# Performance work log

Measured on AMD Instinct MI355X. Metric: run time of the kernel, lower is better.

## Reference

```python
import jax, jax.numpy as jnp
import numpy as np

S, W, V, E, P, PD, H = 2048, 96, 100000, 100, 4096, 50, 100


def setup_inputs() -> dict:
    key = jax.random.key(0)
    ks = jax.random.split(key, 12)
    # small scale (0.05) on params keeps sigmoid/tanh out of saturation
    return {
        "x": jax.random.randint(ks[0], (S, W), 0, V, dtype=jnp.int64) if jax.config.read("jax_enable_x64") else jax.random.randint(ks[0], (S, W), 0, V, dtype=jnp.int32),
        "word_emb": jax.random.normal(ks[1], (V, E), jnp.float32) * 0.05,
        "pos_emb": jax.random.normal(ks[2], (P, PD), jnp.float32) * 0.05,
        "fc1_w": jax.random.normal(ks[3], (H, H), jnp.float32) * 0.05,
        "fc1_b": jax.random.normal(ks[4], (H,), jnp.float32) * 0.05,
        "fc2_w": jax.random.normal(ks[5], (H, H), jnp.float32) * 0.05,
        "fc2_b": jax.random.normal(ks[6], (H,), jnp.float32) * 0.05,
        "Wc": jax.random.normal(ks[7], (1, H), jnp.float32) * 0.05,
        "Ws": jax.random.normal(ks[8], (H, H), jnp.float32) * 0.05,
        "Wr": jax.random.normal(ks[9], (H, H), jnp.float32) * 0.05,
        "Wp": jax.random.normal(ks[10], (1, PD), jnp.float32) * 0.05,
        "b": jax.random.normal(ks[11], (1,), jnp.float32) * 0.05,
    }


def reference(x, word_emb, pos_emb, fc1_w, fc1_b, fc2_w, fc2_b, Wc, Ws, Wr, Wp, b):
    # ragged avg pooling: length = count of nonzero tokens; torch slices data[:length]
    lengths = jnp.sum(jnp.sign(x), axis=1)                     # (S,)
    we = word_emb[x]                                           # (S,W,E)
    mask = (jnp.arange(W)[None, :] < lengths[:, None]).astype(we.dtype)
    denom = jnp.maximum(lengths, 1).astype(we.dtype)[:, None]
    sent = (we * mask[..., None]).sum(axis=1) / denom          # (S,E)

    doc_feat = sent.mean(axis=0)                               # (E,)
    doc = jnp.tanh(doc_feat @ fc1_w.T + fc1_b)                 # (H,)

    h = jnp.tanh(sent @ fc2_w.T + fc2_b)                       # (S,H)
    pos = pos_emb[jnp.arange(S)]                               # (S,PD)

    # per-sentence logit pieces independent of recurrent state s
    pre = h @ Wc[0] + (h @ Ws) @ doc + pos @ Wp[0] + b[0]      # (S,)
    hWr = h @ Wr                                               # (S,H)

    def step(s, inp):
        hi, hwri, prei = inp
        logit = prei - hwri @ jnp.tanh(s)
        prob = jax.nn.sigmoid(logit)
        return s + hi * prob, prob

    s0 = jnp.zeros((H,), h.dtype)
    _, probs = jax.lax.scan(step, s0, (h, hWr, pre))
    return probs[:, None]                                      # (S,1)
```

## Files before the change

kernel.cpp:

```cpp
#include <hip/hip_runtime.h>
#include <hip/hip_bf16.h>

#define S 2048
#define W 96
#define E 100
#define H 100
#define PD 50

typedef float f32x4 __attribute__((ext_vector_type(4)));

__device__ __forceinline__ float fast_rcp(float x) { return __builtin_amdgcn_rcpf(x); }

template<int CTRL, int RM, bool BND>
__device__ __forceinline__ float dpp_add(float x) {
    int t = __builtin_amdgcn_update_dpp(0, __float_as_int(x), CTRL, RM, 0xf, BND);
    return x + __int_as_float(t);
}

__device__ __forceinline__ float wave_sum_bcast(float x) {
    x = dpp_add<0x111, 0xf, true >(x);
    x = dpp_add<0x112, 0xf, true >(x);
    x = dpp_add<0x114, 0xf, true >(x);
    x = dpp_add<0x118, 0xf, true >(x);
    x = dpp_add<0x142, 0xa, false>(x);
    x = dpp_add<0x143, 0xc, false>(x);
    return __int_as_float(__builtin_amdgcn_readlane(__float_as_int(x), 63));
}

__global__ __launch_bounds__(128) void k_sent(const int* __restrict__ x,
                                              const float* __restrict__ word_emb,
                                              float* __restrict__ sent,
                                              float* __restrict__ doc_sum) {
    __shared__ int toks[W];
    __shared__ int s_len;
    const int i = blockIdx.x, t = threadIdx.x;
    if (t == 0) s_len = 0;
    __syncthreads();
    if (t < W) {
        int tok = x[i * W + t];
        toks[t] = tok;
        if (tok > 0) atomicAdd(&s_len, 1);
    }
    __syncthreads();
    const int len = s_len;
    if (t < E) {
        float acc = 0.0f;
        for (int j = 0; j < len; ++j)
            acc += word_emb[toks[j] * E + t];
        float val = acc / (float)max(len, 1);
        sent[i * E + t] = val;
        atomicAdd(&doc_sum[t], val * (1.0f / (float)S));
    }
}

__global__ __launch_bounds__(128) void k_doc(const float* __restrict__ doc_sum,
                                             const float* __restrict__ fc1_w,
                                             const float* __restrict__ fc1_b,
                                             const float* __restrict__ Wc,
                                             const float* __restrict__ Ws,
                                             float* __restrict__ cvec) {
    __shared__ float s_df[E];
    __shared__ float s_doc[H];
    const int t = threadIdx.x;
    if (t < E) s_df[t] = doc_sum[t];
    __syncthreads();
    if (t < H) {
        float acc = fc1_b[t];
        for (int k = 0; k < E; ++k) acc += s_df[k] * fc1_w[t * E + k];
        s_doc[t] = tanhf(acc);
    }
    __syncthreads();
    if (t < H) {
        float c = Wc[t];
        for (int j = 0; j < H; ++j) c += Ws[t * H + j] * s_doc[j];
        cvec[t] = c;
    }
}

__global__ __launch_bounds__(128) void k_row(const float* __restrict__ sent,
                                             const float* __restrict__ fc2_w,
                                             const float* __restrict__ fc2_b,
                                             const float* __restrict__ Wr,
                                             const float* __restrict__ cvec,
                                             const float* __restrict__ pos_emb,
                                             const float* __restrict__ Wp,
                                             const float* __restrict__ bptr,
                                             float* __restrict__ packed) {
    __shared__ float s_sent[E];
    __shared__ float s_h[H];
    __shared__ float red[128];
    const int i = blockIdx.x, t = threadIdx.x;
    float* row = packed + (size_t)i * 256;
    if (t < E) s_sent[t] = sent[i * E + t];
    __syncthreads();
    float hv = 0.0f;
    if (t < H) {
        float acc = fc2_b[t];
        for (int k = 0; k < E; ++k) acc += s_sent[k] * fc2_w[t * E + k];
        hv = tanhf(acc);
        s_h[t] = hv;
    }
    __syncthreads();
    {
        const int m = t >> 1, o = (t & 1) * 2;
        if (t < H) {
            float acc = 0.0f;
            for (int k = 0; k < H; ++k) acc += s_h[k] * Wr[k * H + t];
            row[m * 4 + o]     = 1.44269504f * acc;
            row[m * 4 + o + 1] = hv;
        } else {
            if (t != 100) row[m * 4 + o] = 0.0f;
            row[m * 4 + o + 1] = 0.0f;
        }
    }
    float p = 0.0f;
    if (t < H) p = hv * cvec[t];
    if (t < PD) p += pos_emb[i * PD + t] * Wp[t];
    red[t] = p;
    __syncthreads();
    for (int m = 64; m > 0; m >>= 1) {
        if (t < m) red[t] += red[t + m];
        __syncthreads();
    }
    if (t == 0) row[200] = -1.44269504f * (red[0] + bptr[0]);
}

__global__ __launch_bounds__(64, 1) void k_scan(const f32x4* __restrict__ packed,
                                                float* __restrict__ out) {
    const int l = threadIdx.x;
    const f32x4* pf = packed + l;
    const float mq = (l == 50) ? 1.0f : 0.0f;

    float t0 = 0.0f, t1 = 0.0f, probbuf = 0.0f;

    f32x4 x0, x1, x2, x3, x4, x5, x6, x7;
    f32x4 y0, y1, y2, y3, y4, y5, y6, y7;

#define SB() __builtin_amdgcn_sched_barrier(0)
#define ISSUE(AR, PTR) \
    asm volatile("global_load_dwordx4 %0, %1, off" : "=v"(AR) : "v"(PTR))
#define ISSUE8(P0, P1, P2, P3, P4, P5, P6, P7)                                \
    SB();                                                                     \
    ISSUE(P0, pf + 0 * 64); ISSUE(P1, pf + 1 * 64);                           \
    ISSUE(P2, pf + 2 * 64); ISSUE(P3, pf + 3 * 64);                           \
    ISSUE(P4, pf + 4 * 64); ISSUE(P5, pf + 5 * 64);                           \
    ISSUE(P6, pf + 6 * 64); ISSUE(P7, pf + 7 * 64);                           \
    pf += 8 * 64;                                                             \
    SB();
#define WAIT_ALL()                                                            \
    SB();                                                                     \
    asm volatile("s_waitcnt vmcnt(0)" ::: "memory");                          \
    SB();

#define STEP(CA_, IDX, G)                                                     \
    {                                                                         \
                 \
        float part = fmaf(t0, CA_.x, fmaf(t1, CA_.z, mq * CA_.x));            \
        float total = wave_sum_bcast(part);    \
        float e2 = exp2f(total);                                              \
        float prob = fast_rcp(1.0f + e2);                                     \
         \
        float d0 = CA_.y * prob, d1 = CA_.w * prob;                           \
        float u0 = d0 * d0, u1 = d1 * d1;                                     \
        float T0 = d0 * fmaf(u0, fmaf(u0, 0.13333334f, -0.33333334f), 1.0f);  \
        float T1 = d1 * fmaf(u1, fmaf(u1, 0.13333334f, -0.33333334f), 1.0f);  \
        float r0 = fast_rcp(fmaf(t0, T0, 1.0f));                              \
        float r1 = fast_rcp(fmaf(t1, T1, 1.0f));                              \
        t0 = (t0 + T0) * r0;                                                  \
        t1 = (t1 + T1) * r1;                                                  \
        probbuf = (l == ((G + IDX) & 63)) ? prob : probbuf;                   \
    }
#define COMPUTE8(P0, P1, P2, P3, P4, P5, P6, P7, G)                           \
    STEP(P0, 0, G) STEP(P1, 1, G) STEP(P2, 2, G) STEP(P3, 3, G)               \
    STEP(P4, 4, G) STEP(P5, 5, G) STEP(P6, 6, G) STEP(P7, 7, G)               \
    if (((G) & 63) == 56) out[((G) & ~63) + l] = probbuf;

    ISSUE8(x0, x1, x2, x3, x4, x5, x6, x7)
    WAIT_ALL()

    for (int base = 0; base < S; base += 16) {
        ISSUE8(y0, y1, y2, y3, y4, y5, y6, y7)
        COMPUTE8(x0, x1, x2, x3, x4, x5, x6, x7, base)
        WAIT_ALL()
        ISSUE8(x0, x1, x2, x3, x4, x5, x6, x7)
        COMPUTE8(y0, y1, y2, y3, y4, y5, y6, y7, base + 8)
        WAIT_ALL()
    }
#undef COMPUTE8
#undef STEP
#undef WAIT_ALL
#undef ISSUE8
#undef ISSUE
#undef SB
}

extern "C" void kernel_launch(void* const* d_in, const int* in_sizes, int n_in,
                              void* d_out, int out_size, void* d_ws, size_t ws_size,
                              hipStream_t stream) {
    const int*   x        = (const int*)  d_in[0];
    const float* word_emb = (const float*)d_in[1];
    const float* pos_emb  = (const float*)d_in[2];
    const float* fc1_w    = (const float*)d_in[3];
    const float* fc1_b    = (const float*)d_in[4];
    const float* fc2_w    = (const float*)d_in[5];
    const float* fc2_b    = (const float*)d_in[6];
    const float* Wc       = (const float*)d_in[7];
    const float* Ws       = (const float*)d_in[8];
    const float* Wr       = (const float*)d_in[9];
    const float* Wp       = (const float*)d_in[10];
    const float* bptr     = (const float*)d_in[11];
    float* out = (float*)d_out;

    float* wsf      = (float*)d_ws;
    float* doc_sum  = wsf;
    float* cvec     = wsf + 128;
    float* sent     = wsf + 256;
    float* packed   = sent + S * E;

    hipMemsetAsync(doc_sum, 0, E * sizeof(float), stream);
    hipMemsetAsync(packed + (size_t)S * 256, 0, 16 * 256 * sizeof(float), stream);
    k_sent<<<S, 128, 0, stream>>>(x, word_emb, sent, doc_sum);
    k_doc<<<1, 128, 0, stream>>>(doc_sum, fc1_w, fc1_b, Wc, Ws, cvec);
    k_row<<<S, 128, 0, stream>>>(sent, fc2_w, fc2_b, Wr, cvec, pos_emb, Wp, bptr, packed);
    k_scan<<<1, 64, 0, stream>>>((const f32x4*)packed, out);
}
```

Baseline: 332.7 us.

## Break scan dependency with two-step lookahead linearized logit prediction

Restructures the serial scan so the wave reductions for step i+1 and i+2 are computed one step ahead. The next logit is formed from precomputed reduced terms plus first-order corrections in the current and previous probabilities, taking the cross-lane reduction off the critical path between consecutive steps. It also shortens the tanh series to two terms, stores 1+e2 and inverts once per store, and adds a mid-block vmcnt wait so the lookahead can read the next batch's registers. This trades exactness for a linearized approximation of tanh's derivative and lower-order tanh, which adds numerical risk. The extra wait also reduces overlap of the loads.

```diff
diff --git a/kernel.cpp b/kernel.cpp
--- a/kernel.cpp
+++ b/kernel.cpp
@@ -129,22 +129,25 @@
                                                 float* __restrict__ out) {
     const int l = threadIdx.x;
     const f32x4* pf = packed + l;
-    const float mq = (l == 50) ? 1.0f : 0.0f;
-
-    float t0 = 0.0f, t1 = 0.0f, probbuf = 0.0f;
-
-    f32x4 x0, x1, x2, x3, x4, x5, x6, x7;
-    f32x4 y0, y1, y2, y3, y4, y5, y6, y7;
+
+    float t0 = (l == 50) ? 1.0f : 0.0f;
+    float t1 = 0.0f, probbuf = 1.0f;
+    float p1 = 0.0f, p2 = 0.0f;
+    float hp0 = 0.0f, hp1 = 0.0f;
+    float aE, bE, cE, aO, bO, cO;
+
+    f32x4 a0, a1, a2, a3, a4, a5, a6, a7;
+    f32x4 b0, b1, b2, b3, b4, b5, b6, b7;
 
 #define SB() __builtin_amdgcn_sched_barrier(0)
 #define ISSUE(AR, PTR) \
     asm volatile("global_load_dwordx4 %0, %1, off" : "=v"(AR) : "v"(PTR))
-#define ISSUE8(P0, P1, P2, P3, P4, P5, P6, P7)                                \
+#define ISSUE8(R0, R1, R2, R3, R4, R5, R6, R7)                                \
     SB();                                                                     \
-    ISSUE(P0, pf + 0 * 64); ISSUE(P1, pf + 1 * 64);                           \
-    ISSUE(P2, pf + 2 * 64); ISSUE(P3, pf + 3 * 64);                           \
-    ISSUE(P4, pf + 4 * 64); ISSUE(P5, pf + 5 * 64);                           \
-    ISSUE(P6, pf + 6 * 64); ISSUE(P7, pf + 7 * 64);                           \
+    ISSUE(R0, pf + 0 * 64); ISSUE(R1, pf + 1 * 64);                           \
+    ISSUE(R2, pf + 2 * 64); ISSUE(R3, pf + 3 * 64);                           \
+    ISSUE(R4, pf + 4 * 64); ISSUE(R5, pf + 5 * 64);                           \
+    ISSUE(R6, pf + 6 * 64); ISSUE(R7, pf + 7 * 64);                           \
     pf += 8 * 64;                                                             \
     SB();
 #define WAIT_ALL()                                                            \
@@ -152,41 +155,75 @@
     asm volatile("s_waitcnt vmcnt(0)" ::: "memory");                          \
     SB();
 
-#define STEP(CA_, IDX, G)                                                     \
+#define STEP(CUR, NXT, WP2, AX, BX, CX, IDX, G)                               \
     {                                                                         \
-                 \
-        float part = fmaf(t0, CA_.x, fmaf(t1, CA_.z, mq * CA_.x));            \
-        float total = wave_sum_bcast(part);    \
-        float e2 = exp2f(total);                                              \
-        float prob = fast_rcp(1.0f + e2);                                     \
-         \
-        float d0 = CA_.y * prob, d1 = CA_.w * prob;                           \
+                                    \
+        float tot = fmaf(p1, CX, fmaf(p2, BX, AX));                           \
+        float e2 = exp2f(tot);                                                \
+        float av = e2 + 1.0f;                                                 \
+        float pj = fast_rcp(av);                                              \
+             \
+        float d0 = hp0 * p1, d1 = hp1 * p1;                                   \
         float u0 = d0 * d0, u1 = d1 * d1;                                     \
-        float T0 = d0 * fmaf(u0, fmaf(u0, 0.13333334f, -0.33333334f), 1.0f);  \
-        float T1 = d1 * fmaf(u1, fmaf(u1, 0.13333334f, -0.33333334f), 1.0f);  \
-        float r0 = fast_rcp(fmaf(t0, T0, 1.0f));                              \
-        float r1 = fast_rcp(fmaf(t1, T1, 1.0f));                              \
-        t0 = (t0 + T0) * r0;                                                  \
-        t1 = (t1 + T1) * r1;                                                  \
-        probbuf = (l == ((G + IDX) & 63)) ? prob : probbuf;                   \
-    }
-#define COMPUTE8(P0, P1, P2, P3, P4, P5, P6, P7, G)                           \
-    STEP(P0, 0, G) STEP(P1, 1, G) STEP(P2, 2, G) STEP(P3, 3, G)               \
-    STEP(P4, 4, G) STEP(P5, 5, G) STEP(P6, 6, G) STEP(P7, 7, G)               \
-    if (((G) & 63) == 56) out[((G) & ~63) + l] = probbuf;
-
-    ISSUE8(x0, x1, x2, x3, x4, x5, x6, x7)
+        float T0 = d0 * fmaf(u0, -0.33333334f, 1.0f);                         \
+        float T1 = d1 * fmaf(u1, -0.33333334f, 1.0f);                         \
+        float dM0 = fmaf(t0, T0, 1.0f), dM1 = fmaf(t1, T1, 1.0f);             \
+        t0 = (t0 + T0) * fast_rcp(dM0);                                       \
+        t1 = (t1 + T1) * fast_rcp(dM1);                                       \
+                      \
+        float om0 = fmaf(-t0, t0, 1.0f), om1 = fmaf(-t1, t1, 1.0f);           \
+        float gB0 = CUR.y * om0, gB1 = CUR.w * om1;                           \
+        float gC0 = NXT.y * om0, gC1 = NXT.w * om1;                           \
+        float pA = fmaf(t0, WP2.x, t1 * WP2.z);                               \
+        float pB = fmaf(gB0, WP2.x, gB1 * WP2.z);                             \
+        float pC = fmaf(gC0, WP2.x, gC1 * WP2.z);                             \
+        AX = wave_sum_bcast(pA);                                              \
+        BX = wave_sum_bcast(pB);                                              \
+        CX = wave_sum_bcast(pC);                                              \
+        hp0 = CUR.y; hp1 = CUR.w;                                             \
+        p2 = p1; p1 = pj;                                                     \
+        probbuf = (l == ((G + IDX) & 63)) ? av : probbuf;                     \
+    }
+#define MIDWAIT()                                                             \
+    SB();                                                                     \
+    asm volatile("s_waitcnt vmcnt(0)" ::: "memory");                          \
+    SB();
+#define COMPUTE8(R0, R1, R2, R3, R4, R5, R6, R7, Q0, Q1, G)                   \
+    STEP(R0, R1, R2, aE, bE, cE, 0, G)                                        \
+    STEP(R1, R2, R3, aO, bO, cO, 1, G)                                        \
+    STEP(R2, R3, R4, aE, bE, cE, 2, G)                                        \
+    STEP(R3, R4, R5, aO, bO, cO, 3, G)                                        \
+    STEP(R4, R5, R6, aE, bE, cE, 4, G)                                        \
+    STEP(R5, R6, R7, aO, bO, cO, 5, G)                                        \
+    MIDWAIT()                                                                 \
+    STEP(R6, R7, Q0, aE, bE, cE, 6, G)                                        \
+    STEP(R7, Q0, Q1, aO, bO, cO, 7, G)                                        \
+    if (((G) & 63) == 56) out[((G) & ~63) + l] = fast_rcp(probbuf);
+
+    ISSUE8(a0, a1, a2, a3, a4, a5, a6, a7)
     WAIT_ALL()
 
+    {
+        float pA0 = fmaf(t0, a0.x, t1 * a0.z);
+        aE = wave_sum_bcast(pA0);  bE = 0.0f;  cE = 0.0f;
+        float pA1 = fmaf(t0, a1.x, t1 * a1.z);
+        aO = wave_sum_bcast(pA1);  bO = 0.0f;
+        float om0 = fmaf(-t0, t0, 1.0f), om1 = fmaf(-t1, t1, 1.0f);
+        float g0 = a0.y * om0, g1 = a0.w * om1;
+        float pC1 = fmaf(g0, a1.x, g1 * a1.z);
+        cO = wave_sum_bcast(pC1);
+    }
+
     for (int base = 0; base < S; base += 16) {
-        ISSUE8(y0, y1, y2, y3, y4, y5, y6, y7)
-        COMPUTE8(x0, x1, x2, x3, x4, x5, x6, x7, base)
+        ISSUE8(b0, b1, b2, b3, b4, b5, b6, b7)
+        COMPUTE8(a0, a1, a2, a3, a4, a5, a6, a7, b0, b1, base)
         WAIT_ALL()
-        ISSUE8(x0, x1, x2, x3, x4, x5, x6, x7)
-        COMPUTE8(y0, y1, y2, y3, y4, y5, y6, y7, base + 8)
+        ISSUE8(a0, a1, a2, a3, a4, a5, a6, a7)
+        COMPUTE8(b0, b1, b2, b3, b4, b5, b6, b7, a0, a1, base + 8)
         WAIT_ALL()
     }
 #undef COMPUTE8
+#undef MIDWAIT
 #undef STEP
 #undef WAIT_ALL
 #undef ISSUE8
```

Result: slower. 470.4 us (+41.4%).
